# Optimization experiments

Measured on AMD Instinct MI355X. Metric: run time of the kernel, lower is better.

The kernel has to match this reference:

```python
import jax, jax.numpy as jnp
import numpy as np

N = 100000
IN_C = 128
OUT_C = 128
HEADS = 4
C = OUT_C // HEADS  # per-head channels = 32
E = 1600000
EPS_BN = 1e-5
NEG_SLOPE = 0.2


def setup_inputs() -> dict:
    key = jax.random.key(0)
    ks = jax.random.split(key, 16)
    x = jax.random.normal(ks[0], (N, IN_C), dtype=jnp.float32)
    edge_index = jax.random.randint(ks[1], (2, E), 0, N, dtype=jnp.int64)
    s = 0.05
    params = {
        'W1': jax.random.normal(ks[2], (IN_C, HEADS * C), jnp.float32) * s,
        'a_src1': jax.random.normal(ks[3], (HEADS, C), jnp.float32) * s,
        'a_dst1': jax.random.normal(ks[4], (HEADS, C), jnp.float32) * s,
        'b1': jax.random.normal(ks[5], (HEADS * C,), jnp.float32) * s,
        'gamma1': jnp.ones((OUT_C,), jnp.float32),
        'beta1': jnp.zeros((OUT_C,), jnp.float32),
        'W2': jax.random.normal(ks[6], (OUT_C, HEADS * C), jnp.float32) * s,
        'a_src2': jax.random.normal(ks[7], (HEADS, C), jnp.float32) * s,
        'a_dst2': jax.random.normal(ks[8], (HEADS, C), jnp.float32) * s,
        'b2': jax.random.normal(ks[9], (HEADS * C,), jnp.float32) * s,
        'gamma2': jnp.ones((OUT_C,), jnp.float32),
        'beta2': jnp.zeros((OUT_C,), jnp.float32),
    }
    return {'x': x, 'edge_index': edge_index, **params}


def _gat_conv(x, src, dst, W, a_src, a_dst, b):
    # x: [N, F_in]; src/dst: [E'] (self-loops already appended)
    n = x.shape[0]
    h = (x @ W).reshape(n, HEADS, C)                      # [N, H, C]
    alpha_s = jnp.sum(h * a_src, axis=-1)                 # [N, H]
    alpha_d = jnp.sum(h * a_dst, axis=-1)                 # [N, H]
    logits = alpha_s[src] + alpha_d[dst]                  # [E', H]
    logits = jnp.where(logits >= 0, logits, NEG_SLOPE * logits)
    # segment softmax over incoming edges of each destination node
    m = jax.ops.segment_max(logits, dst, num_segments=n)  # [N, H]
    e = jnp.exp(logits - m[dst])
    denom = jax.ops.segment_sum(e, dst, num_segments=n)   # [N, H]
    alpha = e / (denom[dst] + 1e-16)                      # [E', H]
    msg = alpha[:, :, None] * h[src]                      # [E', H, C]
    out = jax.ops.segment_sum(msg, dst, num_segments=n)   # [N, H, C]
    return out.reshape(n, HEADS * C) + b


def _batch_norm(h, gamma, beta):
    mean = jnp.mean(h, axis=0)
    var = jnp.var(h, axis=0)
    return (h - mean) * jax.lax.rsqrt(var + EPS_BN) * gamma + beta


def reference(x, edge_index, W1, a_src1, a_dst1, b1, gamma1, beta1,
              W2, a_src2, a_dst2, b2, gamma2, beta2):
    # PyG GATConv default: add self-loops
    loops = jnp.arange(N, dtype=edge_index.dtype)
    src = jnp.concatenate([edge_index[0], loops])
    dst = jnp.concatenate([edge_index[1], loops])

    out = _gat_conv(x, src, dst, W1, a_src1, a_dst1, b1)
    out = jax.nn.relu(_batch_norm(out, gamma1, beta1))
    out = _gat_conv(out, src, dst, W2, a_src2, a_dst2, b2)
    out = _batch_norm(out, gamma2, beta2)
    return jax.nn.relu(out + x)  # skip is Identity since in_channels == out_channels
```

## Files before the change

kernel.cpp:

```cpp
#include <hip/hip_runtime.h>

#define MAXNB 1024
#define NSLOT 8

typedef __attribute__((ext_vector_type(8))) short bf8;
typedef __attribute__((ext_vector_type(4))) float f32x4;

__device__ __forceinline__ unsigned pack_bf16x2(float a, float b) {
  unsigned ua = __float_as_uint(a);
  ua = (ua + 0x7fffu + ((ua >> 16) & 1u)) >> 16;
  unsigned ub = __float_as_uint(b);
  ub = (ub + 0x7fffu + ((ub >> 16) & 1u)) >> 16;
  return ua | (ub << 16);
}

__global__ __launch_bounds__(256) void k_wprep(const float* __restrict__ W1,
                                               uint4* __restrict__ Wf1,
                                               const float* __restrict__ W2,
                                               uint4* __restrict__ Wf2) {
  const int half = blockIdx.x >> 3;
  const float* W = half ? W2 : W1;
  uint4* Wf = half ? Wf2 : Wf1;
  const int t = (blockIdx.x & 7) * 256 + threadIdx.x;
  const int frag = t >> 6, lane = t & 63;
  const int ct = frag >> 2, kc = frag & 3;
  const int col = ct * 16 + (lane & 15);
  const int k0 = kc * 32 + (lane >> 4) * 8;
  unsigned p[4];
#pragma unroll
  for (int j = 0; j < 4; ++j)
    p[j] = pack_bf16x2(W[(k0 + 2 * j) * 128 + col],
                       W[(k0 + 2 * j + 1) * 128 + col]);
  Wf[t] = make_uint4(p[0], p[1], p[2], p[3]);
}

__global__ __launch_bounds__(256) void k_gemm(
    const float* __restrict__ X, const uint4* __restrict__ Wf,
    unsigned* __restrict__ Hb, int n, const float* __restrict__ stats,
    const float* __restrict__ gamma, const float* __restrict__ beta,
    float invN, const float* __restrict__ a_src,
    const float* __restrict__ a_dst, float* __restrict__ as_,
    float* __restrict__ ad_) {
  __shared__ float stag[64 * 132];
  __shared__ float ssl[256];
  const int tid = threadIdx.x;
  if (stats && tid < 128) {
    float s = 0.f, s2 = 0.f;
#pragma unroll
    for (int k = 0; k < NSLOT; ++k) {
      s += stats[k * 256 + tid];
      s2 += stats[k * 256 + 128 + tid];
    }
    float mean = s * invN;
    float var = s2 * invN - mean * mean;
    float sc = gamma[tid] * rsqrtf(var + 1e-5f);
    ssl[tid] = sc;
    ssl[128 + tid] = beta[tid] - mean * sc;
  }
  __syncthreads();

  const int w = tid >> 6, lane = tid & 63;
  const int q = lane >> 4, nl = lane & 15;
  const long row0 = (long)blockIdx.x * 64;
  long rowA = row0 + w * 16 + nl;
  if (rowA >= n) rowA = n - 1;

  bf8 a[4];
#pragma unroll
  for (int kc = 0; kc < 4; ++kc) {
    const float* p = X + rowA * 128 + kc * 32 + q * 8;
    float4 v0 = *(const float4*)p;
    float4 v1 = *(const float4*)(p + 4);
    if (stats) {
      const int kb = kc * 32 + q * 8;
      float4 s0 = *(const float4*)&ssl[kb];
      float4 s1 = *(const float4*)&ssl[kb + 4];
      float4 h0 = *(const float4*)&ssl[128 + kb];
      float4 h1 = *(const float4*)&ssl[128 + kb + 4];
      v0.x = fmaxf(fmaf(v0.x, s0.x, h0.x), 0.f);
      v0.y = fmaxf(fmaf(v0.y, s0.y, h0.y), 0.f);
      v0.z = fmaxf(fmaf(v0.z, s0.z, h0.z), 0.f);
      v0.w = fmaxf(fmaf(v0.w, s0.w, h0.w), 0.f);
      v1.x = fmaxf(fmaf(v1.x, s1.x, h1.x), 0.f);
      v1.y = fmaxf(fmaf(v1.y, s1.y, h1.y), 0.f);
      v1.z = fmaxf(fmaf(v1.z, s1.z, h1.z), 0.f);
      v1.w = fmaxf(fmaf(v1.w, s1.w, h1.w), 0.f);
    }
    union { uint4 u; bf8 v; } cv;
    cv.u = make_uint4(pack_bf16x2(v0.x, v0.y), pack_bf16x2(v0.z, v0.w),
                      pack_bf16x2(v1.x, v1.y), pack_bf16x2(v1.z, v1.w));
    a[kc] = cv.v;
  }

  f32x4 acc[8];
#pragma unroll
  for (int ct = 0; ct < 8; ++ct) {
    f32x4 c = {0.f, 0.f, 0.f, 0.f};
#pragma unroll
    for (int kc = 0; kc < 4; ++kc) {
      union { uint4 u; bf8 v; } b;
      b.u = Wf[(ct * 4 + kc) * 64 + lane];
      c = __builtin_amdgcn_mfma_f32_16x16x32_bf16(a[kc], b.v, c, 0, 0, 0);
    }
    acc[ct] = c;
  }

  const int lr = w * 16 + q * 4;
#pragma unroll
  for (int ct = 0; ct < 8; ++ct)
#pragma unroll
    for (int r = 0; r < 4; ++r)
      stag[(lr + r) * 132 + ct * 16 + nl] = acc[ct][r];
  __syncthreads();

  {
    const int row = tid >> 2, seg = tid & 3;
    const long grow = row0 + row;
    if (grow < n) {
      float sp = 0.f, dp = 0.f;
      const float* p = &stag[row * 132 + seg * 32];
#pragma unroll
      for (int i = 0; i < 8; ++i) {
        float4 h4 = *(const float4*)(p + i * 4);
        float4 s4 = ((const float4*)a_src)[seg * 8 + i];
        float4 d4 = ((const float4*)a_dst)[seg * 8 + i];
        sp += h4.x * s4.x + h4.y * s4.y + h4.z * s4.z + h4.w * s4.w;
        dp += h4.x * d4.x + h4.y * d4.y + h4.z * d4.z + h4.w * d4.w;
        uint2 o;
        o.x = pack_bf16x2(h4.x, h4.y);
        o.y = pack_bf16x2(h4.z, h4.w);
        ((uint2*)Hb)[grow * 32 + seg * 8 + i] = o;
      }
      as_[grow * 4 + seg] = sp;
      ad_[grow * 4 + seg] = dp;
    }
  }
}

__global__ __launch_bounds__(256) void k_hist(const int* __restrict__ ei,
                                              int E, int NB,
                                              int* __restrict__ bcnt) {
  __shared__ int hist[MAXNB];
  for (int i = threadIdx.x; i < NB; i += 256) hist[i] = 0;
  __syncthreads();
  const int e0 = blockIdx.x * 4096;
#pragma unroll
  for (int k = 0; k < 16; ++k) {
    int e = e0 + k * 256 + threadIdx.x;
    if (e < E) atomicAdd(&hist[ei[E + e] >> 7], 1);
  }
  __syncthreads();
  for (int i = threadIdx.x; i < NB; i += 256) {
    int c = hist[i];
    if (c) atomicAdd(&bcnt[i], c);
  }
}

__global__ __launch_bounds__(1024) void k_bprefix(const int* __restrict__ bcnt,
                                                  int NB,
                                                  int* __restrict__ bstart,
                                                  int* __restrict__ bcur) {
  __shared__ int sh[1024];
  const int t = threadIdx.x;
  int v = (t < NB) ? bcnt[t] : 0;
  sh[t] = v;
  __syncthreads();
  for (int off = 1; off < 1024; off <<= 1) {
    int u = (t >= off) ? sh[t - off] : 0;
    __syncthreads();
    sh[t] += u;
    __syncthreads();
  }
  if (t < NB) {
    int ex = sh[t] - v;
    bstart[t] = ex;
    bcur[t] = ex;
    if (t == NB - 1) bstart[NB] = sh[t];
  }
}

__global__ __launch_bounds__(256) void k_scatter(const int* __restrict__ ei,
                                                 int E, int NB,
                                                 int* __restrict__ bcur,
                                                 int* __restrict__ packed) {
  __shared__ int hist[MAXNB];
  __shared__ int hbase[MAXNB];
  for (int i = threadIdx.x; i < NB; i += 256) hist[i] = 0;
  __syncthreads();
  const int e0 = blockIdx.x * 4096;
  int myb[16], myv[16];
#pragma unroll
  for (int k = 0; k < 16; ++k) {
    int e = e0 + k * 256 + threadIdx.x;
    myb[k] = -1;
    myv[k] = 0;
    if (e < E) {
      int s = ei[e], d = ei[E + e];
      myb[k] = d >> 7;
      myv[k] = (s << 7) | (d & 127);
      atomicAdd(&hist[myb[k]], 1);
    }
  }
  __syncthreads();
  for (int i = threadIdx.x; i < NB; i += 256) {
    int c = hist[i];
    hbase[i] = c ? atomicAdd(&bcur[i], c) : 0;
    hist[i] = 0;
  }
  __syncthreads();
#pragma unroll
  for (int k = 0; k < 16; ++k) {
    if (myb[k] >= 0) {
      int p = hbase[myb[k]] + atomicAdd(&hist[myb[k]], 1);
      packed[p] = myv[k];
    }
  }
}

__global__ __launch_bounds__(256) void k_local(const int* __restrict__ packed,
                                               const int* __restrict__ bstart,
                                               int n, int* __restrict__ srcs,
                                               int* __restrict__ offs,
                                               int* __restrict__ deg) {
  const int b = blockIdx.x;
  const int node0 = b << 7;
  const int nn = min(128, n - node0);
  const int e0 = bstart[b], e1 = bstart[b + 1];
  __shared__ int dcnt[128], cur[128], scan[128];
  const int tid = threadIdx.x;
  if (tid < 128) dcnt[tid] = 0;
  __syncthreads();
  for (int i = e0 + tid; i < e1; i += 256)
    atomicAdd(&dcnt[packed[i] & 127], 1);
  __syncthreads();
  int v = 0;
  if (tid < 128) {
    v = (tid < nn) ? dcnt[tid] + 1 : 0;
    scan[tid] = v;
  }
  __syncthreads();
  for (int off = 1; off < 128; off <<= 1) {
    int u = 0;
    if (tid < 128 && tid >= off) u = scan[tid - off];
    __syncthreads();
    if (tid < 128) scan[tid] += u;
    __syncthreads();
  }
  if (tid < nn) {
    const int o = e0 + node0 + (scan[tid] - v);
    offs[node0 + tid] = o;
    deg[node0 + tid] = dcnt[tid];
    srcs[o] = node0 + tid;
    cur[tid] = o + 1;
  }
  __syncthreads();
  for (int i = e0 + tid; i < e1; i += 256) {
    const int pv = packed[i];
    const int p = atomicAdd(&cur[pv & 127], 1);
    srcs[p] = pv >> 7;
  }
}

__global__ __launch_bounds__(256) void k_agg(
    const int* __restrict__ offs, const int* __restrict__ deg,
    const int* __restrict__ srcs, const uint4* __restrict__ Hb,
    const float* __restrict__ as_, const float* __restrict__ ad_,
    float* __restrict__ out, float* __restrict__ stats, int n) {
  __shared__ float sblk[4][2][128];
  const int tid = threadIdx.x;
  const int node = blockIdx.x * 16 + (tid >> 4);
  const bool active = node < n;
  const int w = tid >> 6, lane = tid & 63;
  const int t = lane & 15;
  const int th = t >> 2;
  const int j4 = lane & 3;
  const int o0 = active ? offs[node] : 0;
  const int dg = active ? deg[node] + 1 : 0;
  const float adv = active ? ad_[node * 4 + th] : 0.f;

  float den = 0.f;
  float acc[8];
#pragma unroll
  for (int i = 0; i < 8; ++i) acc[i] = 0.f;

  int s = 0;
  float e = 0.f;
  if (j4 < dg) {
    s = srcs[o0 + j4];
    float l = as_[s * 4 + th] + adv;
    l = l >= 0.f ? l : 0.2f * l;
    e = __expf(fminf(l, 80.f));
  }

  for (int base = 0; base < dg; base += 4) {
    int s2 = 0;
    float e2 = 0.f;
    const int jn = base + 4 + j4;
    if (jn < dg) {
      s2 = srcs[o0 + jn];
      float l = as_[s2 * 4 + th] + adv;
      l = l >= 0.f ? l : 0.2f * l;
      e2 = __expf(fminf(l, 80.f));
    }
    den += e;
#pragma unroll
    for (int jj = 0; jj < 4; ++jj) {
      if (base + jj >= dg) break;
      const int ss = __shfl(s, (lane & 48) | jj, 64);
      const float wv = __shfl(e, (lane & ~3) | jj, 64);
      const uint4 hv = Hb[(long)ss * 16 + t];
      acc[0] = fmaf(wv, __uint_as_float(hv.x << 16), acc[0]);
      acc[1] = fmaf(wv, __uint_as_float(hv.x & 0xffff0000u), acc[1]);
      acc[2] = fmaf(wv, __uint_as_float(hv.y << 16), acc[2]);
      acc[3] = fmaf(wv, __uint_as_float(hv.y & 0xffff0000u), acc[3]);
      acc[4] = fmaf(wv, __uint_as_float(hv.z << 16), acc[4]);
      acc[5] = fmaf(wv, __uint_as_float(hv.z & 0xffff0000u), acc[5]);
      acc[6] = fmaf(wv, __uint_as_float(hv.w << 16), acc[6]);
      acc[7] = fmaf(wv, __uint_as_float(hv.w & 0xffff0000u), acc[7]);
    }
    s = s2;
    e = e2;
  }
  den += __shfl_xor(den, 1, 64);
  den += __shfl_xor(den, 2, 64);
  const float invden = 1.f / (den + 1e-16f);
  float sums[8], sqs[8];
#pragma unroll
  for (int i = 0; i < 8; ++i) {
    float v = acc[i] * invden;
    acc[i] = v;
    sums[i] = v;
    sqs[i] = v * v;
  }
  if (active) {
    float4 o0v = make_float4(acc[0], acc[1], acc[2], acc[3]);
    float4 o1v = make_float4(acc[4], acc[5], acc[6], acc[7]);
    ((float4*)out)[(long)node * 32 + t * 2] = o0v;
    ((float4*)out)[(long)node * 32 + t * 2 + 1] = o1v;
  }
#pragma unroll
  for (int off = 16; off <= 32; off <<= 1) {
#pragma unroll
    for (int i = 0; i < 8; ++i) {
      sums[i] += __shfl_xor(sums[i], off, 64);
      sqs[i] += __shfl_xor(sqs[i], off, 64);
    }
  }
  if (lane < 16) {
#pragma unroll
    for (int i = 0; i < 8; ++i) {
      sblk[w][0][lane * 8 + i] = sums[i];
      sblk[w][1][lane * 8 + i] = sqs[i];
    }
  }
  __syncthreads();
  {
    const int c = tid & 127, sidx = tid >> 7;
    float v = sblk[0][sidx][c] + sblk[1][sidx][c] + sblk[2][sidx][c] +
              sblk[3][sidx][c];
    atomicAdd(&stats[(blockIdx.x & (NSLOT - 1)) * 256 + sidx * 128 + c], v);
  }
}

__global__ __launch_bounds__(256) void k_bn_apply(
    const float* __restrict__ V, const float* __restrict__ stats,
    const float* __restrict__ gamma, const float* __restrict__ beta,
    float invN, const float* __restrict__ skip, float* __restrict__ Y,
    int total4) {
  __shared__ float ssl[256];
  const int tid = threadIdx.x;
  if (tid < 128) {
    float s = 0.f, s2 = 0.f;
#pragma unroll
    for (int k = 0; k < NSLOT; ++k) {
      s += stats[k * 256 + tid];
      s2 += stats[k * 256 + 128 + tid];
    }
    float mean = s * invN;
    float var = s2 * invN - mean * mean;
    float sc = gamma[tid] * rsqrtf(var + 1e-5f);
    ssl[tid] = sc;
    ssl[128 + tid] = beta[tid] - mean * sc;
  }
  __syncthreads();
  for (int i = blockIdx.x * 256 + tid; i < total4; i += gridDim.x * 256) {
    const int c4 = i & 31;
    float4 v = ((const float4*)V)[i];
    float4 sc = *(const float4*)&ssl[c4 * 4];
    float4 sh = *(const float4*)&ssl[128 + c4 * 4];
    float4 s = ((const float4*)skip)[i];
    float4 y;
    y.x = fmaxf(fmaf(v.x, sc.x, sh.x) + s.x, 0.f);
    y.y = fmaxf(fmaf(v.y, sc.y, sh.y) + s.y, 0.f);
    y.z = fmaxf(fmaf(v.z, sc.z, sh.z) + s.z, 0.f);
    y.w = fmaxf(fmaf(v.w, sc.w, sh.w) + s.w, 0.f);
    ((float4*)Y)[i] = y;
  }
}

extern "C" void kernel_launch(void* const* d_in, const int* in_sizes, int n_in,
                              void* d_out, int out_size, void* d_ws,
                              size_t ws_size, hipStream_t stream) {
  const float* x = (const float*)d_in[0];
  const int* ei = (const int*)d_in[1];
  const float* W1 = (const float*)d_in[2];
  const float* a_src1 = (const float*)d_in[3];
  const float* a_dst1 = (const float*)d_in[4];
  const float* gamma1 = (const float*)d_in[6];
  const float* beta1 = (const float*)d_in[7];
  const float* W2 = (const float*)d_in[8];
  const float* a_src2 = (const float*)d_in[9];
  const float* a_dst2 = (const float*)d_in[10];
  const float* gamma2 = (const float*)d_in[12];
  const float* beta2 = (const float*)d_in[13];

  const int n = in_sizes[0] / 128;
  const int E = in_sizes[1] / 2;
  const int EP = E + n;
  const int NB = (n + 127) >> 7;
  const int EB = (E + 4095) / 4096;
  const float invN = 1.0f / (float)n;

  char* w = (char*)d_ws;
  const size_t szNC = (size_t)n * 128 * sizeof(float);
  unsigned* Hb = (unsigned*)w;  w += (size_t)n * 64 * sizeof(unsigned);
  float* Bagg = (float*)w;      w += szNC;
  float* as_ = (float*)w;       w += (size_t)n * 4 * sizeof(float);
  float* ad_ = (float*)w;       w += (size_t)n * 4 * sizeof(float);
  int* srcs = (int*)w;          w += (size_t)EP * sizeof(int);
  int* packed = (int*)w;        w += (size_t)E * sizeof(int);
  int* deg = (int*)w;           w += (size_t)n * sizeof(int);
  int* offs = (int*)w;          w += (size_t)n * sizeof(int);
  int* bstart = (int*)w;        w += (size_t)(NB + 1) * sizeof(int);
  int* bcur = (int*)w;          w += (size_t)NB * sizeof(int);
  uint4* Wf1 = (uint4*)w;       w += 2048 * sizeof(uint4);
  uint4* Wf2 = (uint4*)w;       w += 2048 * sizeof(uint4);
  char* zreg = w;
  int* bcnt = (int*)w;          w += (size_t)NB * sizeof(int);
  float* stats1 = (float*)w;    w += NSLOT * 256 * sizeof(float);
  float* stats2 = (float*)w;    w += NSLOT * 256 * sizeof(float);
  const size_t zbytes = (size_t)(w - zreg);

  hipMemsetAsync(zreg, 0, zbytes, stream);

  k_wprep<<<16, 256, 0, stream>>>(W1, Wf1, W2, Wf2);

  k_hist<<<EB, 256, 0, stream>>>(ei, E, NB, bcnt);
  k_bprefix<<<1, 1024, 0, stream>>>(bcnt, NB, bstart, bcur);
  k_scatter<<<EB, 256, 0, stream>>>(ei, E, NB, bcur, packed);
  k_local<<<NB, 256, 0, stream>>>(packed, bstart, n, srcs, offs, deg);

  k_gemm<<<(n + 63) / 64, 256, 0, stream>>>(x, Wf1, Hb, n, nullptr, nullptr,
                                            nullptr, invN, a_src1, a_dst1,
                                            as_, ad_);
  k_agg<<<(n + 15) / 16, 256, 0, stream>>>(offs, deg, srcs, (const uint4*)Hb,
                                           as_, ad_, Bagg, stats1, n);

  k_gemm<<<(n + 63) / 64, 256, 0, stream>>>(Bagg, Wf2, Hb, n, stats1, gamma1,
                                            beta1, invN, a_src2, a_dst2, as_,
                                            ad_);
  k_agg<<<(n + 15) / 16, 256, 0, stream>>>(offs, deg, srcs, (const uint4*)Hb,
                                           as_, ad_, Bagg, stats2, n);
  k_bn_apply<<<2048, 256, 0, stream>>>(Bagg, stats2, gamma2, beta2, invN, x,
                                       (float*)d_out, n * 32);
}
```

Measured before the change: 456.2 us.

## Sort destination nodes by in-degree to balance aggregation work across wavefronts

Adds a degree histogram, scan and permutation pass so the aggregation kernels process nodes grouped by similar in-degree, reducing divergence where 16-lane groups in a wave wait on the longest neighbor list. It also folds the workspace memset into the weight-prep kernel as an extra block and raises the number of BN stats slots. The cost is three extra small launches, an indirect node lookup, and scattered output writes and destination reads in aggregation.

```diff
diff --git a/kernel.cpp b/kernel.cpp
--- a/kernel.cpp
+++ b/kernel.cpp
@@ -1,7 +1,8 @@
 #include <hip/hip_runtime.h>
 
 #define MAXNB 1024
-#define NSLOT 8
+#define NSLOT 32
+#define DBINS 64
 
 typedef __attribute__((ext_vector_type(8))) short bf8;
 typedef __attribute__((ext_vector_type(4))) float f32x4;
@@ -14,10 +15,16 @@
   return ua | (ub << 16);
 }
 
-__global__ __launch_bounds__(256) void k_wprep(const float* __restrict__ W1,
-                                               uint4* __restrict__ Wf1,
-                                               const float* __restrict__ W2,
-                                               uint4* __restrict__ Wf2) {
+__global__ __launch_bounds__(256) void k_prep(const float* __restrict__ W1,
+                                              uint4* __restrict__ Wf1,
+                                              const float* __restrict__ W2,
+                                              uint4* __restrict__ Wf2,
+                                              int* __restrict__ zreg,
+                                              int zwords) {
+  if (blockIdx.x == 16) {
+    for (int i = threadIdx.x; i < zwords; i += 256) zreg[i] = 0;
+    return;
+  }
   const int half = blockIdx.x >> 3;
   const float* W = half ? W2 : W1;
   uint4* Wf = half ? Wf2 : Wf1;
@@ -261,15 +268,65 @@
   }
 }
 
+__global__ __launch_bounds__(1024) void k_dhist(const int* __restrict__ deg,
+                                                int n, int* __restrict__ dbin) {
+  __shared__ int h[DBINS];
+  if (threadIdx.x < DBINS) h[threadIdx.x] = 0;
+  __syncthreads();
+  const int i = blockIdx.x * 1024 + threadIdx.x;
+  if (i < n) atomicAdd(&h[min(deg[i], DBINS - 1)], 1);
+  __syncthreads();
+  if (threadIdx.x < DBINS && h[threadIdx.x])
+    atomicAdd(&dbin[threadIdx.x], h[threadIdx.x]);
+}
+
+__global__ void k_dscan(const int* __restrict__ dbin, int* __restrict__ dcur) {
+  __shared__ int sh[DBINS];
+  const int t = threadIdx.x;
+  int v = dbin[t];
+  sh[t] = v;
+  __syncthreads();
+  for (int off = 1; off < DBINS; off <<= 1) {
+    int u = (t >= off) ? sh[t - off] : 0;
+    __syncthreads();
+    sh[t] += u;
+    __syncthreads();
+  }
+  dcur[t] = sh[t] - v;
+}
+
+__global__ __launch_bounds__(256) void k_dperm(const int* __restrict__ deg,
+                                               int n, int* __restrict__ dcur,
+                                               int* __restrict__ perm) {
+  __shared__ int h[DBINS], base[DBINS];
+  if (threadIdx.x < DBINS) h[threadIdx.x] = 0;
+  __syncthreads();
+  const int i = blockIdx.x * 256 + threadIdx.x;
+  int d = 0, loc = 0;
+  if (i < n) {
+    d = min(deg[i], DBINS - 1);
+    loc = atomicAdd(&h[d], 1);
+  }
+  __syncthreads();
+  if (threadIdx.x < DBINS) {
+    int c = h[threadIdx.x];
+    base[threadIdx.x] = c ? atomicAdd(&dcur[threadIdx.x], c) : 0;
+  }
+  __syncthreads();
+  if (i < n) perm[base[d] + loc] = i;
+}
+
 __global__ __launch_bounds__(256) void k_agg(
-    const int* __restrict__ offs, const int* __restrict__ deg,
-    const int* __restrict__ srcs, const uint4* __restrict__ Hb,
-    const float* __restrict__ as_, const float* __restrict__ ad_,
-    float* __restrict__ out, float* __restrict__ stats, int n) {
+    const int* __restrict__ perm, const int* __restrict__ offs,
+    const int* __restrict__ deg, const int* __restrict__ srcs,
+    const uint4* __restrict__ Hb, const float* __restrict__ as_,
+    const float* __restrict__ ad_, float* __restrict__ out,
+    float* __restrict__ stats, int n) {
   __shared__ float sblk[4][2][128];
   const int tid = threadIdx.x;
-  const int node = blockIdx.x * 16 + (tid >> 4);
-  const bool active = node < n;
+  const int gid = blockIdx.x * 16 + (tid >> 4);
+  const bool active = gid < n;
+  const int node = active ? perm[gid] : 0;
   const int w = tid >> 6, lane = tid & 63;
   const int t = lane & 15;
   const int th = t >> 2;
@@ -431,36 +488,43 @@
   int* packed = (int*)w;        w += (size_t)E * sizeof(int);
   int* deg = (int*)w;           w += (size_t)n * sizeof(int);
   int* offs = (int*)w;          w += (size_t)n * sizeof(int);
+  int* perm = (int*)w;          w += (size_t)n * sizeof(int);
   int* bstart = (int*)w;        w += (size_t)(NB + 1) * sizeof(int);
   int* bcur = (int*)w;          w += (size_t)NB * sizeof(int);
+  int* dcur = (int*)w;          w += DBINS * sizeof(int);
   uint4* Wf1 = (uint4*)w;       w += 2048 * sizeof(uint4);
   uint4* Wf2 = (uint4*)w;       w += 2048 * sizeof(uint4);
   char* zreg = w;
   int* bcnt = (int*)w;          w += (size_t)NB * sizeof(int);
+  int* dbin = (int*)w;          w += DBINS * sizeof(int);
   float* stats1 = (float*)w;    w += NSLOT * 256 * sizeof(float);
   float* stats2 = (float*)w;    w += NSLOT * 256 * sizeof(float);
-  const size_t zbytes = (size_t)(w - zreg);
-
-  hipMemsetAsync(zreg, 0, zbytes, stream);
-
-  k_wprep<<<16, 256, 0, stream>>>(W1, Wf1, W2, Wf2);
+  const int zwords = (int)((w - zreg) / sizeof(int));
+
+  k_prep<<<17, 256, 0, stream>>>(W1, Wf1, W2, Wf2, (int*)zreg, zwords);
 
   k_hist<<<EB, 256, 0, stream>>>(ei, E, NB, bcnt);
   k_bprefix<<<1, 1024, 0, stream>>>(bcnt, NB, bstart, bcur);
   k_scatter<<<EB, 256, 0, stream>>>(ei, E, NB, bcur, packed);
   k_local<<<NB, 256, 0, stream>>>(packed, bstart, n, srcs, offs, deg);
 
+  k_dhist<<<(n + 1023) / 1024, 1024, 0, stream>>>(deg, n, dbin);
+  k_dscan<<<1, DBINS, 0, stream>>>(dbin, dcur);
+  k_dperm<<<(n + 255) / 256, 256, 0, stream>>>(deg, n, dcur, perm);
+
   k_gemm<<<(n + 63) / 64, 256, 0, stream>>>(x, Wf1, Hb, n, nullptr, nullptr,
                                             nullptr, invN, a_src1, a_dst1,
                                             as_, ad_);
-  k_agg<<<(n + 15) / 16, 256, 0, stream>>>(offs, deg, srcs, (const uint4*)Hb,
-                                           as_, ad_, Bagg, stats1, n);
+  k_agg<<<(n + 15) / 16, 256, 0, stream>>>(perm, offs, deg, srcs,
+                                           (const uint4*)Hb, as_, ad_, Bagg,
+                                           stats1, n);
 
   k_gemm<<<(n + 63) / 64, 256, 0, stream>>>(Bagg, Wf2, Hb, n, stats1, gamma1,
                                             beta1, invN, a_src2, a_dst2, as_,
                                             ad_);
-  k_agg<<<(n + 15) / 16, 256, 0, stream>>>(offs, deg, srcs, (const uint4*)Hb,
-                                           as_, ad_, Bagg, stats2, n);
+  k_agg<<<(n + 15) / 16, 256, 0, stream>>>(perm, offs, deg, srcs,
+                                           (const uint4*)Hb, as_, ad_, Bagg,
+                                           stats2, n);
   k_bn_apply<<<2048, 256, 0, stream>>>(Bagg, stats2, gamma2, beta2, invN, x,
                                        (float*)d_out, n * 32);
 }
```

Result: slower. 466.8 us (+2.3%).
